# Kernel optimization log

Measured on AMD Instinct MI355X. Metric: run time of the kernel, lower is better.

## Reference

```python
import jax, jax.numpy as jnp
import numpy as np

# Static video grid (F, H, W); S = F*H*W tokens.
F_FRAMES, H_GRID, W_GRID = 9, 16, 28
DIM, N_HEADS = 1536, 12
HEAD_DIM = DIM // N_HEADS          # 128
ROT = HEAD_DIM // 2                # 64 complex pairs
EPS = 1e-6


def setup_inputs() -> dict:
    key = jax.random.key(0)
    ks = jax.random.split(key, 12)
    S = F_FRAMES * H_GRID * W_GRID
    scale = 0.02
    inp = {
        "x": jax.random.normal(ks[0], (1, S, DIM), jnp.float32),
        "seq_lens": jnp.array([S], jnp.int32),
        "grid_sizes": jnp.array([[F_FRAMES, H_GRID, W_GRID]], jnp.int32),
        "freqs": jax.random.normal(ks[1], (1024, ROT), jnp.float32),  # rope angles
        "Wq": jax.random.normal(ks[2], (DIM, DIM), jnp.float32) * scale,
        "bq": jnp.zeros((DIM,), jnp.float32),
        "Wk": jax.random.normal(ks[3], (DIM, DIM), jnp.float32) * scale,
        "bk": jnp.zeros((DIM,), jnp.float32),
        "Wv": jax.random.normal(ks[4], (DIM, DIM), jnp.float32) * scale,
        "bv": jnp.zeros((DIM,), jnp.float32),
        "Wo": jax.random.normal(ks[5], (DIM, DIM), jnp.float32) * scale,
        "bo": jnp.zeros((DIM,), jnp.float32),
        "gq": jnp.ones((DIM,), jnp.float32),
        "gk": jnp.ones((DIM,), jnp.float32),
    }
    return inp


def _rms_norm(h, g):
    # WanRMSNorm: h * rsqrt(mean(h^2) + eps) * weight
    var = jnp.mean(jnp.square(h), axis=-1, keepdims=True)
    return h * jax.lax.rsqrt(var + EPS) * g


def _rope_angles(freqs):
    # Split channel dim into temporal / height / width parts.
    c = ROT
    t_dim = c - 2 * (c // 3)  # 22
    s1 = c // 3               # 21
    temporal, height, width = freqs[:, :t_dim], freqs[:, t_dim:t_dim + s1], freqs[:, t_dim + s1:]
    t_ang = jnp.repeat(temporal[:F_FRAMES], H_GRID * W_GRID, axis=0)         # [S, 22]
    h_ang = jnp.tile(jnp.repeat(height[:H_GRID], W_GRID, axis=0), (F_FRAMES, 1))  # [S, 21]
    w_ang = jnp.tile(jnp.tile(width[:W_GRID], (H_GRID, 1)), (F_FRAMES, 1))        # [S, 21]
    return jnp.concatenate([t_ang, h_ang, w_ang], axis=-1)  # [S, c]


def _rope_apply(x, ang):
    # x: [B, S, n, d] viewed as complex pairs [B, S, n, d/2, 2]
    b, s, n, d = x.shape
    xp = x.reshape(b, s, n, d // 2, 2)
    xr, xi = xp[..., 0], xp[..., 1]
    cos = jnp.cos(ang)[None, :, None, :]
    sin = jnp.sin(ang)[None, :, None, :]
    out_r = xr * cos - xi * sin
    out_i = xr * sin + xi * cos
    return jnp.stack([out_r, out_i], axis=-1).reshape(b, s, n, d)


def reference(x, seq_lens, grid_sizes, freqs, Wq, bq, Wk, bk, Wv, bv, Wo, bo, gq, gk):
    b, s, _ = x.shape
    n, d = N_HEADS, HEAD_DIM
    q = _rms_norm(x @ Wq + bq, gq).reshape(b, s, n, d)
    k = _rms_norm(x @ Wk + bk, gk).reshape(b, s, n, d)
    v = (x @ Wv + bv).reshape(b, s, n, d)

    ang = _rope_angles(freqs)  # [S, d/2]
    rq = _rope_apply(q, ang)
    rk = _rope_apply(k, ang)

    # Causal frame-block mask: query in frame i attends to kv in frames <= i.
    frame_idx = jnp.arange(s) // (H_GRID * W_GRID)
    mask = frame_idx[None, :] <= frame_idx[:, None]  # [S_q, S_k]

    scale = 1.0 / jnp.sqrt(jnp.asarray(d, x.dtype))
    scores = jnp.einsum("bqnd,bknd->bnqk", rq, rk) * scale
    scores = jnp.where(mask[None, None], scores, jnp.asarray(-1e30, scores.dtype))
    probs = jax.nn.softmax(scores, axis=-1)
    attn = jnp.einsum("bnqk,bknd->bqnd", probs, v).reshape(b, s, n * d)
    return attn @ Wo + bo
```

## Files before the change

kernel.cpp:

```cpp
#include <hip/hip_runtime.h>
#include <stdint.h>

typedef unsigned short u16;
typedef unsigned int u32;
typedef __attribute__((ext_vector_type(8))) short bf16x8;
typedef __attribute__((ext_vector_type(4))) float f32x4;

#define S_LEN 4032
#define S_PAD 4096
#define DIMC  1536
#define HD    128
#define FRAME 448

static const size_t OFF_FLAG  = 0;
static const size_t OFF_CANON = 256;
static const size_t OFF_XB    = 524288;
static const size_t OFF_WT    = OFF_XB  + 12582912;
static const size_t OFF_WOT   = OFF_WT  + 14155776;
static const size_t OFF_YQ    = OFF_WOT + 4718592;
static const size_t OFF_YK    = OFF_YQ  + 12582912;
static const size_t OFF_VT    = OFF_YK  + 12582912;
static const size_t OFF_QH    = OFF_VT  + 12582912;
static const size_t OFF_KH    = OFF_QH  + 12386304;
static const size_t OFF_AT    = OFF_KH  + 12386304;
static const size_t WS_NEED   = OFF_AT  + 12582912;

#define C_BQ 0
#define C_BO 4608
#define C_GQ 6144
#define C_GK 7680
#define C_FR 9216
#define C_TOT 74752

__device__ __forceinline__ u16 f2bf(float f) {
  union { float f; u32 u; } v; v.f = f;
  u32 u = v.u;
  u32 r = (u + 0x7fffu + ((u >> 16) & 1u)) >> 16;
  return (u16)r;
}
__device__ __forceinline__ float bf2f(u16 h) {
  union { float f; u32 u; } v; v.u = ((u32)h) << 16;
  return v.f;
}

__device__ __forceinline__ void gld_lds16(const void* g, void* l) {
  __builtin_amdgcn_global_load_lds(
      (const __attribute__((address_space(1))) void*)(uintptr_t)g,
      (__attribute__((address_space(3))) void*)(u32)(uintptr_t)l,
      16, 0, 0);
}

__device__ __forceinline__ f32x4 mfma16(bf16x8 a, bf16x8 b, f32x4 c) {
  return __builtin_amdgcn_mfma_f32_16x16x32_bf16(a, b, c, 0, 0, 0);
}

__global__ void prep_all(const void* __restrict__ x,
                         const void* Wq, const void* Wk, const void* Wv, const void* Wo,
                         const void* bq, const void* bk, const void* bv, const void* bo,
                         const void* gq, const void* gk, const void* fr,
                         float* __restrict__ canon, u16* __restrict__ xb,
                         u16* __restrict__ wqkvt, u16* __restrict__ wot,
                         int* __restrict__ flag) {
  __shared__ int cnt;
  __shared__ float tile[32][33];
  const int tid = threadIdx.x;
  if (tid == 0) cnt = 0;
  __syncthreads();
  int e = (((const u16*)x)[2 * tid] >> 7) & 0xff;
  if (e > 150) atomicAdd(&cnt, 1);
  __syncthreads();
  const int fl = (cnt >= 8) ? 1 : 0;
  const int bid = blockIdx.x;
  if (bid == 0 && tid == 0) *flag = fl;

  if (bid < 9216) {
    const int z = bid / 2304;
    const int rem = bid % 2304;
    const int by = rem / 48, bx = rem % 48;
    const void* W = (z == 0) ? Wq : (z == 1) ? Wk : (z == 2) ? Wv : Wo;
    u16* dst = (z < 3) ? (wqkvt + (size_t)z * DIMC * DIMC) : wot;
    const int tx = tid & 31, ty = tid >> 5;
    const int c = bx * 32 + tx;
    #pragma unroll
    for (int i = 0; i < 4; i++) {
      int r = by * 32 + ty + i * 8;
      float v = fl ? ((const float*)W)[(size_t)r * DIMC + c]
                   : bf2f(((const u16*)W)[(size_t)r * DIMC + c]);
      tile[ty + i * 8][tx] = v;
    }
    __syncthreads();
    const int k = by * 32 + tx;
    #pragma unroll
    for (int i = 0; i < 4; i++) {
      int n = bx * 32 + ty + i * 8;
      dst[(size_t)n * DIMC + k] = f2bf(tile[tx][ty + i * 8]);
    }
  } else if (bid < 12288) {
    int i = (bid - 9216) * 256 + tid;
    if (i < (S_PAD * DIMC) / 8) {
      size_t base = (size_t)i * 8;
      int row = (int)(base / DIMC);
      union { u16 h[8]; uint4 v; } u;
      if (row < S_LEN) {
        if (fl) {
          const float* xf = (const float*)x + base;
          #pragma unroll
          for (int j = 0; j < 8; j++) u.h[j] = f2bf(xf[j]);
        } else {
          const u16* xh = (const u16*)x + base;
          #pragma unroll
          for (int j = 0; j < 8; j++) u.h[j] = xh[j];
        }
      } else {
        #pragma unroll
        for (int j = 0; j < 8; j++) u.h[j] = 0;
      }
      ((uint4*)xb)[i] = u.v;
    }
  } else {
    for (int i = (bid - 12288) * 256 + tid; i < C_TOT; i += 292 * 256) {
      const void* src; int j;
      if      (i < 1536) { src = bq; j = i; }
      else if (i < 3072) { src = bk; j = i - 1536; }
      else if (i < 4608) { src = bv; j = i - 3072; }
      else if (i < 6144) { src = bo; j = i - 4608; }
      else if (i < 7680) { src = gq; j = i - 6144; }
      else if (i < 9216) { src = gk; j = i - 7680; }
      else               { src = fr; j = i - 9216; }
      canon[i] = fl ? ((const float*)src)[j] : bf2f(((const u16*)src)[j]);
    }
  }
}

template <int MODE>
__launch_bounds__(256, 4)
__global__ void gemm_bt(const u16* __restrict__ A, const u16* __restrict__ Bt,
                        const float* __restrict__ canon,
                        u16* __restrict__ Yq, u16* __restrict__ Yk, u16* __restrict__ Vt,
                        void* __restrict__ Out, const int* __restrict__ flagp) {
  const int bm0 = blockIdx.y * 128, bn0 = blockIdx.x * 128;
  const int tid = threadIdx.x, wave = tid >> 6, lane = tid & 63;
  const int wm = wave >> 1, wn = wave & 1;
  const int l15 = lane & 15, l4 = lane >> 4;
  __shared__ u16 sA[128 * 64];
  __shared__ u16 sB[128 * 64];
  f32x4 acc[4][4];
  #pragma unroll
  for (int i = 0; i < 4; i++)
    #pragma unroll
    for (int j = 0; j < 4; j++) acc[i][j] = (f32x4){0.f, 0.f, 0.f, 0.f};

  const int swc = ((lane & 7) ^ (lane >> 3)) * 8;
  const u16* Ab = A  + (size_t)(bm0 + (lane >> 3)) * DIMC + swc;
  const u16* Bb = Bt + (size_t)(bn0 + (lane >> 3)) * DIMC + swc;

  for (int kt = 0; kt < DIMC; kt += 64) {
    __syncthreads();
    #pragma unroll
    for (int c = 0; c < 4; c++) {
      int g = wave * 4 + c;
      gld_lds16(Ab + (size_t)g * 8 * DIMC + kt, (char*)sA + g * 1024);
      gld_lds16(Bb + (size_t)g * 8 * DIMC + kt, (char*)sB + g * 1024);
    }
    __syncthreads();
    #pragma unroll
    for (int ks = 0; ks < 2; ks++) {
      bf16x8 av[4], bvv[4];
      #pragma unroll
      for (int mt = 0; mt < 4; mt++)
        av[mt]  = *(const bf16x8*)(sA + (wm * 64 + mt * 16 + l15) * 64 +
                                   (((ks * 4 + l4) ^ (l15 & 7)) * 8));
      #pragma unroll
      for (int nt = 0; nt < 4; nt++)
        bvv[nt] = *(const bf16x8*)(sB + (wn * 64 + nt * 16 + l15) * 64 +
                                   (((ks * 4 + l4) ^ (l15 & 7)) * 8));
      #pragma unroll
      for (int mt = 0; mt < 4; mt++)
        #pragma unroll
        for (int nt = 0; nt < 4; nt++)
          acc[mt][nt] = mfma16(av[mt], bvv[nt], acc[mt][nt]);
    }
  }

  const int gm0 = bm0 + wm * 64;
  const int gn0 = bn0 + wn * 64;
  if (MODE == 0) {
    #pragma unroll
    for (int nt = 0; nt < 4; nt++) {
      int gn = gn0 + nt * 16 + l15;
      float b = canon[C_BQ + gn];
      #pragma unroll
      for (int mt = 0; mt < 4; mt++) {
        int gm = gm0 + mt * 16 + l4 * 4;
        if (gn < 1536) {
          #pragma unroll
          for (int r = 0; r < 4; r++)
            Yq[(size_t)(gm + r) * DIMC + gn] = f2bf(acc[mt][nt][r] + b);
        } else if (gn < 3072) {
          int g2 = gn - 1536;
          #pragma unroll
          for (int r = 0; r < 4; r++)
            Yk[(size_t)(gm + r) * DIMC + g2] = f2bf(acc[mt][nt][r] + b);
        } else {
          int g2 = gn - 3072;
          u32 lo = (u32)f2bf(acc[mt][nt][0] + b) | ((u32)f2bf(acc[mt][nt][1] + b) << 16);
          u32 hi = (u32)f2bf(acc[mt][nt][2] + b) | ((u32)f2bf(acc[mt][nt][3] + b) << 16);
          uint2 pk; pk.x = lo; pk.y = hi;
          *(uint2*)(Vt + (size_t)g2 * S_PAD + gm) = pk;
        }
      }
    }
  } else {
    const int fl = *flagp;
    #pragma unroll
    for (int nt = 0; nt < 4; nt++) {
      int gn = gn0 + nt * 16 + l15;
      float b = canon[C_BO + gn];
      #pragma unroll
      for (int mt = 0; mt < 4; mt++) {
        int gm = gm0 + mt * 16 + l4 * 4;
        #pragma unroll
        for (int r = 0; r < 4; r++) {
          int gr = gm + r;
          if (gr < S_LEN) {
            float v = acc[mt][nt][r] + b;
            if (fl) ((float*)Out)[(size_t)gr * DIMC + gn] = v;
            else    ((u16*)Out)[(size_t)gr * DIMC + gn] = f2bf(v);
          }
        }
      }
    }
  }
}

__global__ void norm_rope(const u16* __restrict__ Yq, const u16* __restrict__ Yk,
                          const float* __restrict__ canon, u16* __restrict__ Qh,
                          u16* __restrict__ Kh) {
  const int tid = threadIdx.x, wave = tid >> 6, lane = tid & 63;
  const int s = blockIdx.x * 4 + wave;
  const int isq = (blockIdx.y == 0);
  const u16* Y = isq ? Yq : Yk;
  const float* g = canon + (isq ? C_GQ : C_GK);
  u16* Oh = isq ? Qh : Kh;
  const float sc = isq ? (0.08838834764831845f * 1.4426950408889634f) : 1.0f;

  const u32* yrow = (const u32*)Y + (size_t)s * 768;
  float xr[12], xi[12];
  float ss = 0.f;
  #pragma unroll
  for (int i = 0; i < 12; i++) {
    u32 d = yrow[lane + 64 * i];
    float a = bf2f((u16)(d & 0xffff));
    float b = bf2f((u16)(d >> 16));
    xr[i] = a; xi[i] = b;
    ss += a * a + b * b;
  }
  #pragma unroll
  for (int dd = 1; dd < 64; dd <<= 1) ss += __shfl_xor(ss, dd, 64);
  float rms = rsqrtf(ss * (1.f / 1536.f) + 1e-6f);

  int f_ = s / FRAME, hh = (s % FRAME) / 28, ww = s % 28;
  const float* fr = canon + C_FR;
  float a = (lane < 22) ? fr[f_ * 64 + lane]
          : (lane < 43) ? fr[hh * 64 + lane]
                        : fr[ww * 64 + lane];
  float si, co;
  __sincosf(a, &si, &co);

  const float2* g2 = (const float2*)g;
  #pragma unroll
  for (int i = 0; i < 12; i++) {
    int p = lane + 64 * i;
    float2 gg = g2[p];
    float r  = xr[i] * rms * gg.x;
    float im = xi[i] * rms * gg.y;
    u32 pk = (u32)f2bf((r * co - im * si) * sc) | ((u32)f2bf((r * si + im * co) * sc) << 16);
    ((u32*)Oh)[((size_t)i * S_LEN + s) * 64 + lane] = pk;
  }
}

__launch_bounds__(256, 2)
__global__ void attn_v8(const u16* __restrict__ Qh, const u16* __restrict__ Kh,
                        const u16* __restrict__ Vt, u16* __restrict__ Ab) {
  const int tid = threadIdx.x, wave = tid >> 6, lane = tid & 63;
  const int l15 = lane & 15, l4 = lane >> 4;
  const int qh = wave >> 1;
  const int kh = wave & 1;
  const int h = blockIdx.x % 12;
  const int qb = 62 - (blockIdx.x / 12);
  const int q0 = qb * 64;
  const int nkv = (q0 / FRAME + 1) * 7;
  __shared__ u16 sK[2][8192];
  __shared__ u16 sV[2][8192];
  __shared__ u16 sP[4][2][512];

  int koff[4], voff[4];
  #pragma unroll
  for (int i = 0; i < 4; i++) {
    int c = i * 256 + tid;
    int r = c >> 4, cc = (c & 15) ^ (r & 15);
    koff[i] = r * HD + cc * 8;
    int rv = c >> 3, cv = (c & 7) ^ (rv & 7);
    voff[i] = rv * S_PAD + cv * 8;
  }

  bf16x8 qf[4][2];
  {
    const u16* qp = Qh + ((size_t)h * S_LEN + q0 + qh * 32 + l15) * HD + l4 * 8;
    #pragma unroll
    for (int f = 0; f < 2; f++)
      #pragma unroll
      for (int ks = 0; ks < 4; ks++)
        qf[ks][f] = *(const bf16x8*)(qp + f * 16 * HD + ks * 32);
  }
  f32x4 o[8][2];
  #pragma unroll
  for (int i = 0; i < 8; i++)
    #pragma unroll
    for (int f = 0; f < 2; f++) o[i][f] = (f32x4){0.f, 0.f, 0.f, 0.f};
  float l_i[2] = {0.f, 0.f};

  const u16* kb0 = Kh + (size_t)h * S_LEN * HD;
  const u16* vb0 = Vt + (size_t)h * HD * S_PAD;

  #pragma unroll
  for (int i = 0; i < 4; i++) {
    gld_lds16(kb0 + koff[i], (char*)sK[0] + i * 4096 + wave * 1024);
    gld_lds16(vb0 + voff[i], (char*)sV[0] + i * 4096 + wave * 1024);
  }
  __syncthreads();

  for (int t = 0; t < nkv; ++t) {
    const int cur = t & 1;
    if (t + 1 < nkv) {
      const u16* kb = kb0 + (size_t)(t + 1) * 64 * HD;
      const u16* vb = vb0 + (t + 1) * 64;
      #pragma unroll
      for (int i = 0; i < 4; i++) {
        gld_lds16(kb + koff[i], (char*)sK[cur ^ 1] + i * 4096 + wave * 1024);
        gld_lds16(vb + voff[i], (char*)sV[cur ^ 1] + i * 4096 + wave * 1024);
      }
    }

    f32x4 sT[2][2];
    #pragma unroll
    for (int nt = 0; nt < 2; nt++)
      #pragma unroll
      for (int f = 0; f < 2; f++) sT[nt][f] = (f32x4){0.f, 0.f, 0.f, 0.f};
    __builtin_amdgcn_s_setprio(1);
    #pragma unroll
    for (int ks = 0; ks < 4; ks++) {
      bf16x8 kf[2];
      #pragma unroll
      for (int nt = 0; nt < 2; nt++)
        kf[nt] = *(const bf16x8*)(sK[cur] + (kh * 32 + nt * 16 + l15) * HD +
                                  (((ks * 4 + l4) ^ l15) * 8));
      #pragma unroll
      for (int nt = 0; nt < 2; nt++)
        #pragma unroll
        for (int f = 0; f < 2; f++)
          sT[nt][f] = mfma16(kf[nt], qf[ks][f], sT[nt][f]);
    }
    __builtin_amdgcn_s_setprio(0);

    #pragma unroll
    for (int f = 0; f < 2; f++) {
      float rs = 0.f;
      u16* pw = sP[wave][f];
      #pragma unroll
      for (int nt = 0; nt < 2; nt++) {
        #pragma unroll
        for (int r = 0; r < 4; r++) {
          float p = __builtin_amdgcn_exp2f(sT[nt][f][r]);
          sT[nt][f][r] = p; rs += p;
        }
        u32 lo = (u32)f2bf(sT[nt][f][0]) | ((u32)f2bf(sT[nt][f][1]) << 16);
        u32 hi = (u32)f2bf(sT[nt][f][2]) | ((u32)f2bf(sT[nt][f][3]) << 16);
        u32 off = (u32)((nt * 2 + (l4 >> 1)) * 128 + l15 * 8 + (l4 & 1) * 4);
        uint2 pk; pk.x = lo; pk.y = hi;
        *(uint2*)(pw + off) = pk;
      }
      l_i[f] += rs;
    }

    bf16x8 pb[2];
    #pragma unroll
    for (int f = 0; f < 2; f++)
      pb[f] = *(const bf16x8*)(sP[wave][f] + lane * 8);
    __builtin_amdgcn_s_setprio(1);
    #pragma unroll
    for (int vt = 0; vt < 8; vt++) {
      bf16x8 vf = *(const bf16x8*)(sV[cur] + (vt * 16 + l15) * 64 +
                                   (((kh * 4 + l4) ^ (l15 & 7)) * 8));
      #pragma unroll
      for (int f = 0; f < 2; f++)
        o[vt][f] = mfma16(vf, pb[f], o[vt][f]);
    }
    __builtin_amdgcn_s_setprio(0);

    __syncthreads();
  }

  #pragma unroll
  for (int f = 0; f < 2; f++) {
    l_i[f] += __shfl_xor(l_i[f], 16, 64);
    l_i[f] += __shfl_xor(l_i[f], 32, 64);
  }
  float* mb = (float*)sK;
  float* lb = (float*)sP;
  if (kh == 1) {
    #pragma unroll
    for (int f = 0; f < 2; f++) {
      #pragma unroll
      for (int vt = 0; vt < 8; vt++)
        *(f32x4*)(mb + qh * 4096 + (f * 8 + vt) * 256 + lane * 4) = o[vt][f];
      lb[qh * 128 + f * 64 + lane] = l_i[f];
    }
  }
  __syncthreads();
  if (kh == 0) {
    #pragma unroll
    for (int f = 0; f < 2; f++) {
      float l = l_i[f] + lb[qh * 128 + f * 64 + lane];
      float inv = 1.f / l;
      const size_t orow = (size_t)(q0 + qh * 32 + f * 16 + l15) * DIMC + (size_t)h * HD;
      #pragma unroll
      for (int vt = 0; vt < 8; vt++) {
        f32x4 op = *(const f32x4*)(mb + qh * 4096 + (f * 8 + vt) * 256 + lane * 4);
        float o0 = (o[vt][f][0] + op[0]) * inv;
        float o1 = (o[vt][f][1] + op[1]) * inv;
        float o2 = (o[vt][f][2] + op[2]) * inv;
        float o3 = (o[vt][f][3] + op[3]) * inv;
        u32 lo = (u32)f2bf(o0) | ((u32)f2bf(o1) << 16);
        u32 hi = (u32)f2bf(o2) | ((u32)f2bf(o3) << 16);
        uint2 pk; pk.x = lo; pk.y = hi;
        *(uint2*)(Ab + orow + vt * 16 + l4 * 4) = pk;
      }
    }
  }
}

extern "C" void kernel_launch(void* const* d_in, const int* in_sizes, int n_in,
                              void* d_out, int out_size, void* d_ws, size_t ws_size,
                              hipStream_t stream) {
  if (ws_size < WS_NEED) return;
  char* ws = (char*)d_ws;
  int*   flag  = (int*)(ws + OFF_FLAG);
  float* canon = (float*)(ws + OFF_CANON);
  u16* xb    = (u16*)(ws + OFF_XB);
  u16* wqkvt = (u16*)(ws + OFF_WT);
  u16* wot   = (u16*)(ws + OFF_WOT);
  u16* yq    = (u16*)(ws + OFF_YQ);
  u16* yk    = (u16*)(ws + OFF_YK);
  u16* vt    = (u16*)(ws + OFF_VT);
  u16* qh    = (u16*)(ws + OFF_QH);
  u16* kh    = (u16*)(ws + OFF_KH);
  u16* ab    = (u16*)(ws + OFF_AT);

  const void* x  = d_in[0];
  const void* fr = d_in[3];
  const void* Wq = d_in[4];  const void* bq = d_in[5];
  const void* Wk = d_in[6];  const void* bk = d_in[7];
  const void* Wv = d_in[8];  const void* bv = d_in[9];
  const void* Wo = d_in[10]; const void* bo = d_in[11];
  const void* gq = d_in[12]; const void* gk = d_in[13];

  prep_all<<<12580, 256, 0, stream>>>(x, Wq, Wk, Wv, Wo, bq, bk, bv, bo, gq, gk, fr,
                                      canon, xb, wqkvt, wot, flag);
  gemm_bt<0><<<dim3(36, 32), 256, 0, stream>>>(xb, wqkvt, canon, yq, yk, vt, nullptr, flag);
  norm_rope<<<dim3(1008, 2), 256, 0, stream>>>(yq, yk, canon, qh, kh);
  attn_v8<<<756, 256, 0, stream>>>(qh, kh, vt, ab);
  gemm_bt<1><<<dim3(12, 32), 256, 0, stream>>>(ab, wot, canon, nullptr, nullptr, nullptr, d_out, flag);
}
```

Measured before the change: 323.9 us.

## Double-buffer GEMM LDS loads, swizzle tile order, use explicit vmcnt waits

The projection GEMM gets double-buffered LDS tiles, so the next K-slice is prefetched while MFMAs run on the current one. Workgroups are remapped with a modulo-8 swizzle, likely to improve cache locality across XCDs. Both the GEMM and attention loops replace __syncthreads with partial s_waitcnt vmcnt(8) plus raw barriers, so the next tile's loads stay in flight. The GEMM launch bound drops to 2 waves per SIMD because doubled LDS lowers occupancy, and the hand-counted vmcnt waits risk races if the load count changes.

```diff
diff --git a/kernel.cpp b/kernel.cpp
--- a/kernel.cpp
+++ b/kernel.cpp
@@ -53,6 +53,10 @@
 __device__ __forceinline__ f32x4 mfma16(bf16x8 a, bf16x8 b, f32x4 c) {
   return __builtin_amdgcn_mfma_f32_16x16x32_bf16(a, b, c, 0, 0, 0);
 }
+
+#define WAITV8() asm volatile("s_waitcnt vmcnt(8)" ::: "memory")
+#define WAITV0() asm volatile("s_waitcnt vmcnt(0)" ::: "memory")
+#define BAR()    __builtin_amdgcn_s_barrier()
 
 __global__ void prep_all(const void* __restrict__ x,
                          const void* Wq, const void* Wk, const void* Wv, const void* Wo,
@@ -133,17 +137,21 @@
 }
 
 template <int MODE>
-__launch_bounds__(256, 4)
+__launch_bounds__(256, 2)
 __global__ void gemm_bt(const u16* __restrict__ A, const u16* __restrict__ Bt,
                         const float* __restrict__ canon,
                         u16* __restrict__ Yq, u16* __restrict__ Yk, u16* __restrict__ Vt,
                         void* __restrict__ Out, const int* __restrict__ flagp) {
-  const int bm0 = blockIdx.y * 128, bn0 = blockIdx.x * 128;
+  constexpr int nbx = (MODE == 0) ? 36 : 12;
+  constexpr int nwg = nbx * 32;
+  const int bid = blockIdx.x + blockIdx.y * nbx;
+  const int swz = (bid & 7) * (nwg >> 3) + (bid >> 3);
+  const int bm0 = (swz / nbx) * 128, bn0 = (swz % nbx) * 128;
   const int tid = threadIdx.x, wave = tid >> 6, lane = tid & 63;
   const int wm = wave >> 1, wn = wave & 1;
   const int l15 = lane & 15, l4 = lane >> 4;
-  __shared__ u16 sA[128 * 64];
-  __shared__ u16 sB[128 * 64];
+  __shared__ u16 sA[2][128 * 64];
+  __shared__ u16 sB[2][128 * 64];
   f32x4 acc[4][4];
   #pragma unroll
   for (int i = 0; i < 4; i++)
@@ -154,25 +162,38 @@
   const u16* Ab = A  + (size_t)(bm0 + (lane >> 3)) * DIMC + swc;
   const u16* Bb = Bt + (size_t)(bn0 + (lane >> 3)) * DIMC + swc;
 
+  #pragma unroll
+  for (int c = 0; c < 4; c++) {
+    int g = wave * 4 + c;
+    gld_lds16(Ab + (size_t)g * 8 * DIMC, (char*)sA[0] + g * 1024);
+    gld_lds16(Bb + (size_t)g * 8 * DIMC, (char*)sB[0] + g * 1024);
+  }
+
   for (int kt = 0; kt < DIMC; kt += 64) {
-    __syncthreads();
-    #pragma unroll
-    for (int c = 0; c < 4; c++) {
-      int g = wave * 4 + c;
-      gld_lds16(Ab + (size_t)g * 8 * DIMC + kt, (char*)sA + g * 1024);
-      gld_lds16(Bb + (size_t)g * 8 * DIMC + kt, (char*)sB + g * 1024);
-    }
-    __syncthreads();
+    const int cur = (kt >> 6) & 1;
+    if (kt + 64 < DIMC) {
+      #pragma unroll
+      for (int c = 0; c < 4; c++) {
+        int g = wave * 4 + c;
+        gld_lds16(Ab + (size_t)g * 8 * DIMC + kt + 64, (char*)sA[cur ^ 1] + g * 1024);
+        gld_lds16(Bb + (size_t)g * 8 * DIMC + kt + 64, (char*)sB[cur ^ 1] + g * 1024);
+      }
+      WAITV8();
+    } else {
+      WAITV0();
+    }
+    BAR();
+
     #pragma unroll
     for (int ks = 0; ks < 2; ks++) {
       bf16x8 av[4], bvv[4];
       #pragma unroll
       for (int mt = 0; mt < 4; mt++)
-        av[mt]  = *(const bf16x8*)(sA + (wm * 64 + mt * 16 + l15) * 64 +
+        av[mt]  = *(const bf16x8*)(sA[cur] + (wm * 64 + mt * 16 + l15) * 64 +
                                    (((ks * 4 + l4) ^ (l15 & 7)) * 8));
       #pragma unroll
       for (int nt = 0; nt < 4; nt++)
-        bvv[nt] = *(const bf16x8*)(sB + (wn * 64 + nt * 16 + l15) * 64 +
+        bvv[nt] = *(const bf16x8*)(sB[cur] + (wn * 64 + nt * 16 + l15) * 64 +
                                    (((ks * 4 + l4) ^ (l15 & 7)) * 8));
       #pragma unroll
       for (int mt = 0; mt < 4; mt++)
@@ -180,6 +201,7 @@
         for (int nt = 0; nt < 4; nt++)
           acc[mt][nt] = mfma16(av[mt], bvv[nt], acc[mt][nt]);
     }
+    BAR();
   }
 
   const int gm0 = bm0 + wm * 64;
@@ -280,7 +302,7 @@
 }
 
 __launch_bounds__(256, 2)
-__global__ void attn_v8(const u16* __restrict__ Qh, const u16* __restrict__ Kh,
+__global__ void attn_v9(const u16* __restrict__ Qh, const u16* __restrict__ Kh,
                         const u16* __restrict__ Vt, u16* __restrict__ Ab) {
   const int tid = threadIdx.x, wave = tid >> 6, lane = tid & 63;
   const int l15 = lane & 15, l4 = lane >> 4;
@@ -328,7 +350,6 @@
     gld_lds16(kb0 + koff[i], (char*)sK[0] + i * 4096 + wave * 1024);
     gld_lds16(vb0 + voff[i], (char*)sV[0] + i * 4096 + wave * 1024);
   }
-  __syncthreads();
 
   for (int t = 0; t < nkv; ++t) {
     const int cur = t & 1;
@@ -340,7 +361,11 @@
         gld_lds16(kb + koff[i], (char*)sK[cur ^ 1] + i * 4096 + wave * 1024);
         gld_lds16(vb + voff[i], (char*)sV[cur ^ 1] + i * 4096 + wave * 1024);
       }
-    }
+      WAITV8();
+    } else {
+      WAITV0();
+    }
+    BAR();
 
     f32x4 sT[2][2];
     #pragma unroll
@@ -398,7 +423,7 @@
     }
     __builtin_amdgcn_s_setprio(0);
 
-    __syncthreads();
+    BAR();
   }
 
   #pragma unroll
@@ -408,6 +433,7 @@
   }
   float* mb = (float*)sK;
   float* lb = (float*)sP;
+  __syncthreads();
   if (kh == 1) {
     #pragma unroll
     for (int f = 0; f < 2; f++) {
@@ -469,6 +495,6 @@
                                       canon, xb, wqkvt, wot, flag);
   gemm_bt<0><<<dim3(36, 32), 256, 0, stream>>>(xb, wqkvt, canon, yq, yk, vt, nullptr, flag);
   norm_rope<<<dim3(1008, 2), 256, 0, stream>>>(yq, yk, canon, qh, kh);
-  attn_v8<<<756, 256, 0, stream>>>(qh, kh, vt, ab);
+  attn_v9<<<756, 256, 0, stream>>>(qh, kh, vt, ab);
   gemm_bt<1><<<dim3(12, 32), 256, 0, stream>>>(ab, wot, canon, nullptr, nullptr, nullptr, d_out, flag);
 }
```

New measurement: 335.0 us. 3.4% more time.
